# Optimization experiments

Hardware: AMD Instinct MI355X
Metric: run time of the kernel (lower is better)

Reference implementation:

```python
import jax, jax.numpy as jnp
import numpy as np

B, N, DIM = 4, 2048, 512
H, DH = 8, 64  # heads, dim_head; inner_dim = H*DH = 512
SCALE = DH ** -0.5
EPS = 1e-5


def _layer_norm(x, gamma):
    # LayerNorm with learned gamma and beta fixed to zeros (beta is a buffer)
    mu = jnp.mean(x, axis=-1, keepdims=True)
    var = jnp.var(x, axis=-1, keepdims=True)
    return (x - mu) * jax.lax.rsqrt(var + EPS) * gamma


def setup_inputs() -> dict:
    key = jax.random.key(0)
    ks = jax.random.split(key, 6)
    x = jax.random.normal(ks[0], (B, N, DIM), jnp.float32)
    mask = jax.random.bernoulli(ks[1], 0.9, (B, N))  # bool [b, n]
    gamma = jnp.ones((DIM,), jnp.float32)            # pre-attn LayerNorm gamma
    Wq = jax.random.normal(ks[2], (DIM, H * DH), jnp.float32) * 0.02
    Wkv = jax.random.normal(ks[3], (DIM, 2 * DH), jnp.float32) * 0.02  # shared single KV head (MQA)
    null_kv = jax.random.normal(ks[4], (2, DH), jnp.float32)
    Wout = jax.random.normal(ks[5], (H * DH, DIM), jnp.float32) * 0.02
    out_gamma = jnp.ones((DIM,), jnp.float32)        # post-proj LayerNorm gamma
    return {"x": x, "mask": mask, "gamma": gamma, "Wq": Wq, "Wkv": Wkv,
            "null_kv": null_kv, "Wout": Wout, "out_gamma": out_gamma}


def reference(x, mask, gamma, Wq, Wkv, null_kv, Wout, out_gamma):
    b, n, _ = x.shape
    xn = _layer_norm(x, gamma)
    # queries: per-head; keys/values: single shared head (multi-query)
    q = (xn @ Wq).reshape(b, n, H, DH).transpose(0, 2, 1, 3) * SCALE  # [b,h,n,d]
    kv = xn @ Wkv                                                     # [b,n,2d]
    k, v = kv[..., :DH], kv[..., DH:]                                 # [b,n,d]
    # prepend learned null key/value (attention sink) shared across batch
    nk = jnp.broadcast_to(null_kv[0], (b, 1, DH))
    nv = jnp.broadcast_to(null_kv[1], (b, 1, DH))
    k = jnp.concatenate([nk, k], axis=1)  # [b, n+1, d]
    v = jnp.concatenate([nv, v], axis=1)
    sim = jnp.einsum('bhid,bjd->bhij', q, k)  # [b,h,n,n+1]
    # mask padded with True for the null token, broadcast over heads/queries
    m = jnp.concatenate([jnp.ones((b, 1), bool), mask], axis=1)
    max_neg = -jnp.finfo(sim.dtype).max
    sim = jnp.where(m[:, None, None, :], sim, max_neg)
    attn = jax.nn.softmax(sim.astype(jnp.float32), axis=-1).astype(x.dtype)
    out = jnp.einsum('bhij,bjd->bhid', attn, v)       # [b,h,n,d]
    out = out.transpose(0, 2, 1, 3).reshape(b, n, H * DH)
    return _layer_norm(out @ Wout, out_gamma)
```

## Files before the change

### kernel.cpp

```cpp
#include <hip/hip_runtime.h>

typedef __attribute__((ext_vector_type(8)))  short bf16x8;
typedef __attribute__((ext_vector_type(4)))  float f32x4;
typedef __attribute__((ext_vector_type(16))) float f32x16;
typedef __attribute__((ext_vector_type(4)))  unsigned u32x4;

#define Nx 2048
#define CTXx 2049
#define KCAP 2112
#define QSCALE 0.18033688f

__device__ __forceinline__ short f2bs(float x){
    unsigned u = __builtin_bit_cast(unsigned, x);
    u = (u + 0x7fffu + ((u >> 16) & 1u)) >> 16;
    return (short)u;
}
__device__ __forceinline__ unsigned pack_trunc(float a, float b){
    return __builtin_amdgcn_perm(__builtin_bit_cast(unsigned, b),
                                 __builtin_bit_cast(unsigned, a), 0x07060302u);
}

__global__ void __launch_bounds__(256) ln1_prep_kernel(const float* __restrict__ x,
                                                       const float* __restrict__ g,
                                                       short* __restrict__ xnb,
                                                       const float* __restrict__ Wq,
                                                       const float* __restrict__ Wkv,
                                                       const float* __restrict__ Wout,
                                                       const float* __restrict__ nkv,
                                                       short* __restrict__ WcatT,
                                                       short* __restrict__ WoutT,
                                                       short* __restrict__ kb,
                                                       short* __restrict__ vbt){
    __shared__ float ls[64][65];
    int t = threadIdx.x;
    if (blockIdx.x < 2048){
        int w = t >> 6, lane = t & 63;
        size_t row = (size_t)blockIdx.x * 4 + w;
        const float* xr = x + row * 512 + lane * 8;
        float4 a = *(const float4*)xr;
        float4 b = *(const float4*)(xr + 4);
        float s = a.x + a.y + a.z + a.w + b.x + b.y + b.z + b.w;
        float q = a.x*a.x + a.y*a.y + a.z*a.z + a.w*a.w
                + b.x*b.x + b.y*b.y + b.z*b.z + b.w*b.w;
        #pragma unroll
        for (int m = 1; m < 64; m <<= 1){ s += __shfl_xor(s, m, 64); q += __shfl_xor(q, m, 64); }
        float mu  = s * (1.f / 512.f);
        float var = fmaxf(q * (1.f / 512.f) - mu * mu, 0.f);
        float r   = rsqrtf(var + 1e-5f);
        const float* gr = g + lane * 8;
        float4 g0 = *(const float4*)gr;
        float4 g1 = *(const float4*)(gr + 4);
        bf16x8 o;
        o[0] = f2bs((a.x - mu) * r * g0.x); o[1] = f2bs((a.y - mu) * r * g0.y);
        o[2] = f2bs((a.z - mu) * r * g0.z); o[3] = f2bs((a.w - mu) * r * g0.w);
        o[4] = f2bs((b.x - mu) * r * g1.x); o[5] = f2bs((b.y - mu) * r * g1.y);
        o[6] = f2bs((b.z - mu) * r * g1.z); o[7] = f2bs((b.w - mu) * r * g1.w);
        *(bf16x8*)(xnb + row * 512 + lane * 8) = o;
        return;
    }
    int bid = blockIdx.x - 2048;
    if (bid == 144){
        int b = t >> 6, d = t & 63;
        kb[((size_t)b * KCAP) * 64 + d] = f2bs(nkv[d]);
        vbt[((size_t)b * 64 + d) * KCAP + 0] = f2bs(nkv[64 + d]);
        return;
    }
    bool isOut = (bid >= 80);
    int b2 = isOut ? bid - 80 : bid;
    int ntile = isOut ? (b2 & 7) : (b2 % 10);
    int ktile = isOut ? (b2 >> 3) : (b2 / 10);
    int n0 = ntile * 64, k0 = ktile * 64;
    #pragma unroll
    for (int rr = 0; rr < 64; rr += 16){
        int r = rr + (t >> 4), c = (t & 15) * 4;
        float4 v;
        if (isOut)            v = *(const float4*)(Wout + (size_t)(k0 + r) * 512 + n0 + c);
        else if (n0 < 512)    v = *(const float4*)(Wq   + (size_t)(k0 + r) * 512 + n0 + c);
        else                  v = *(const float4*)(Wkv  + (size_t)(k0 + r) * 128 + (n0 - 512) + c);
        ls[c + 0][r] = v.x; ls[c + 1][r] = v.y; ls[c + 2][r] = v.z; ls[c + 3][r] = v.w;
    }
    __syncthreads();
    int rn = t >> 2, kc = (t & 3) * 16;
    short tmp[16];
    #pragma unroll
    for (int j = 0; j < 16; j++) tmp[j] = f2bs(ls[rn][kc + j]);
    short* dst = (isOut ? WoutT : WcatT) + (size_t)(n0 + rn) * 512 + k0 + kc;
    *(int4*)dst       = *(int4*)&tmp[0];
    *(int4*)(dst + 8) = *(int4*)&tmp[8];
}

__global__ void __launch_bounds__(256) ln2_kernel(const float* __restrict__ z,
                                                  const float* __restrict__ g,
                                                  float* __restrict__ out){
    int w = threadIdx.x >> 6, lane = threadIdx.x & 63;
    size_t row = (size_t)blockIdx.x * 4 + w;
    const float* xr = z + row * 512 + lane * 8;
    float4 a = *(const float4*)xr;
    float4 b = *(const float4*)(xr + 4);
    float s = a.x + a.y + a.z + a.w + b.x + b.y + b.z + b.w;
    float q = a.x*a.x + a.y*a.y + a.z*a.z + a.w*a.w
            + b.x*b.x + b.y*b.y + b.z*b.z + b.w*b.w;
    #pragma unroll
    for (int m = 1; m < 64; m <<= 1){ s += __shfl_xor(s, m, 64); q += __shfl_xor(q, m, 64); }
    float mu  = s * (1.f / 512.f);
    float var = fmaxf(q * (1.f / 512.f) - mu * mu, 0.f);
    float r   = rsqrtf(var + 1e-5f);
    const float* gr = g + lane * 8;
    float4 g0 = *(const float4*)gr;
    float4 g1 = *(const float4*)(gr + 4);
    float4 o0, o1;
    o0.x = (a.x - mu) * r * g0.x; o0.y = (a.y - mu) * r * g0.y;
    o0.z = (a.z - mu) * r * g0.z; o0.w = (a.w - mu) * r * g0.w;
    o1.x = (b.x - mu) * r * g1.x; o1.y = (b.y - mu) * r * g1.y;
    o1.z = (b.z - mu) * r * g1.z; o1.w = (b.w - mu) * r * g1.w;
    float* op = out + row * 512 + lane * 8;
    *(float4*)op = o0; *(float4*)(op + 4) = o1;
}

__global__ void __launch_bounds__(256, 1) gemm_qkv(const short* __restrict__ A,
                                                   const short* __restrict__ BwT,
                                                   short* __restrict__ qb,
                                                   short* __restrict__ kb,
                                                   short* __restrict__ vbt){
    __shared__ short As[2][128][72];
    __shared__ short Bs[2][160][72];
    int t = threadIdx.x;
    int lane = t & 63, w = t >> 6;
    int l16 = lane & 15, quad = lane >> 4;
    int wm = w & 1, wn = w >> 1;
    int row0 = blockIdx.y * 128, col0 = blockIdx.x * 160;
    f32x4 acc[4][5];
    #pragma unroll
    for (int i = 0; i < 4; i++)
        #pragma unroll
        for (int j = 0; j < 5; j++) acc[i][j] = (f32x4){0.f, 0.f, 0.f, 0.f};
    int ar = t >> 1, ak = (t & 1) * 32;
    const short* ap = A + (size_t)(row0 + ar) * 512 + ak;
    int4 a0 = *(const int4*)(ap);      int4 a1 = *(const int4*)(ap + 8);
    int4 a2 = *(const int4*)(ap + 16); int4 a3 = *(const int4*)(ap + 24);
    int4 pb[5];
    int brow[5], bseg[5];
    #pragma unroll
    for (int ps = 0; ps < 5; ps++){
        int idx = ps * 256 + t;
        brow[ps] = idx >> 3; bseg[ps] = (idx & 7) * 8;
        pb[ps] = *(const int4*)(BwT + (size_t)(col0 + brow[ps]) * 512 + bseg[ps]);
    }
    int p = 0;
    for (int k0 = 0; k0 < 512; k0 += 64){
        *(int4*)&As[p][ar][ak]      = a0;
        *(int4*)&As[p][ar][ak + 8]  = a1;
        *(int4*)&As[p][ar][ak + 16] = a2;
        *(int4*)&As[p][ar][ak + 24] = a3;
        #pragma unroll
        for (int ps = 0; ps < 5; ps++)
            *(int4*)&Bs[p][brow[ps]][bseg[ps]] = pb[ps];
        __syncthreads();
        int kn = k0 + 64;
        if (kn < 512){
            a0 = *(const int4*)(ap + kn);      a1 = *(const int4*)(ap + kn + 8);
            a2 = *(const int4*)(ap + kn + 16); a3 = *(const int4*)(ap + kn + 24);
            #pragma unroll
            for (int ps = 0; ps < 5; ps++)
                pb[ps] = *(const int4*)(BwT + (size_t)(col0 + brow[ps]) * 512 + kn + bseg[ps]);
        }
        #pragma unroll
        for (int ks = 0; ks < 2; ks++){
            bf16x8 af[4], bfr[5];
            #pragma unroll
            for (int mt = 0; mt < 4; mt++)
                af[mt] = *(const bf16x8*)&As[p][wm * 64 + mt * 16 + l16][ks * 32 + quad * 8];
            #pragma unroll
            for (int nt = 0; nt < 5; nt++)
                bfr[nt] = *(const bf16x8*)&Bs[p][wn * 80 + nt * 16 + l16][ks * 32 + quad * 8];
            #pragma unroll
            for (int mt = 0; mt < 4; mt++)
                #pragma unroll
                for (int nt = 0; nt < 5; nt++)
                    acc[mt][nt] = __builtin_amdgcn_mfma_f32_16x16x32_bf16(af[mt], bfr[nt], acc[mt][nt], 0, 0, 0);
        }
        p ^= 1;
    }
    #pragma unroll
    for (int mt = 0; mt < 4; mt++)
        #pragma unroll
        for (int nt = 0; nt < 5; nt++)
            #pragma unroll
            for (int r = 0; r < 4; r++){
                int row = row0 + wm * 64 + mt * 16 + quad * 4 + r;
                int col = col0 + wn * 80 + nt * 16 + l16;
                float v = acc[mt][nt][r];
                int bb = row >> 11, ii = row & 2047;
                if (col < 512){
                    qb[(size_t)row * 512 + col] = f2bs(v * QSCALE);
                } else if (col < 576){
                    kb[((size_t)bb * KCAP + ii + 1) * 64 + (col - 512)] = f2bs(v);
                } else {
                    vbt[((size_t)bb * 64 + (col - 576)) * KCAP + ii + 1] = f2bs(v);
                }
            }
}

__global__ void __launch_bounds__(256, 2) gemm_out(const short* __restrict__ A,
                                                   const short* __restrict__ BwT,
                                                   float* __restrict__ C){
    __shared__ short As[2][128][72];
    __shared__ short Bs[2][128][72];
    int t = threadIdx.x;
    int lane = t & 63, w = t >> 6;
    int l16 = lane & 15, quad = lane >> 4;
    int wm = w & 1, wn = w >> 1;
    int row0 = blockIdx.y * 128, col0 = blockIdx.x * 128;
    f32x4 acc[4][4];
    #pragma unroll
    for (int i = 0; i < 4; i++)
        #pragma unroll
        for (int j = 0; j < 4; j++) acc[i][j] = (f32x4){0.f, 0.f, 0.f, 0.f};
    int ar = t >> 1, ak = (t & 1) * 32;
    const short* ap = A   + (size_t)(row0 + ar) * 512 + ak;
    const short* bp = BwT + (size_t)(col0 + ar) * 512 + ak;
    int4 a0 = *(const int4*)(ap);      int4 a1 = *(const int4*)(ap + 8);
    int4 a2 = *(const int4*)(ap + 16); int4 a3 = *(const int4*)(ap + 24);
    int4 b0 = *(const int4*)(bp);      int4 b1 = *(const int4*)(bp + 8);
    int4 b2 = *(const int4*)(bp + 16); int4 b3 = *(const int4*)(bp + 24);
    int p = 0;
    for (int k0 = 0; k0 < 512; k0 += 64){
        *(int4*)&As[p][ar][ak]      = a0;
        *(int4*)&As[p][ar][ak + 8]  = a1;
        *(int4*)&As[p][ar][ak + 16] = a2;
        *(int4*)&As[p][ar][ak + 24] = a3;
        *(int4*)&Bs[p][ar][ak]      = b0;
        *(int4*)&Bs[p][ar][ak + 8]  = b1;
        *(int4*)&Bs[p][ar][ak + 16] = b2;
        *(int4*)&Bs[p][ar][ak + 24] = b3;
        __syncthreads();
        int kn = k0 + 64;
        if (kn < 512){
            a0 = *(const int4*)(ap + kn);      a1 = *(const int4*)(ap + kn + 8);
            a2 = *(const int4*)(ap + kn + 16); a3 = *(const int4*)(ap + kn + 24);
            b0 = *(const int4*)(bp + kn);      b1 = *(const int4*)(bp + kn + 8);
            b2 = *(const int4*)(bp + kn + 16); b3 = *(const int4*)(bp + kn + 24);
        }
        #pragma unroll
        for (int ks = 0; ks < 2; ks++){
            bf16x8 af[4], bfr[4];
            #pragma unroll
            for (int mt = 0; mt < 4; mt++)
                af[mt] = *(const bf16x8*)&As[p][wm * 64 + mt * 16 + l16][ks * 32 + quad * 8];
            #pragma unroll
            for (int nt = 0; nt < 4; nt++)
                bfr[nt] = *(const bf16x8*)&Bs[p][wn * 64 + nt * 16 + l16][ks * 32 + quad * 8];
            #pragma unroll
            for (int mt = 0; mt < 4; mt++)
                #pragma unroll
                for (int nt = 0; nt < 4; nt++)
                    acc[mt][nt] = __builtin_amdgcn_mfma_f32_16x16x32_bf16(af[mt], bfr[nt], acc[mt][nt], 0, 0, 0);
        }
        p ^= 1;
    }
    #pragma unroll
    for (int mt = 0; mt < 4; mt++)
        #pragma unroll
        for (int nt = 0; nt < 4; nt++)
            #pragma unroll
            for (int r = 0; r < 4; r++){
                int row = row0 + wm * 64 + mt * 16 + quad * 4 + r;
                int col = col0 + wn * 64 + nt * 16 + l16;
                C[(size_t)row * 512 + col] = acc[mt][nt][r];
            }
}

__global__ void __launch_bounds__(256, 2) attn_kernel(const short* __restrict__ qb,
                                                      const short* __restrict__ kb,
                                                      const short* __restrict__ vbt,
                                                      const int* __restrict__ mask,
                                                      short* __restrict__ ob){
    __shared__ short Ks[2][64][72];
    __shared__ short Vt[2][64][72];
    int t = threadIdx.x;
    int lane = t & 63, w = t >> 6;
    int n32 = lane & 31, hb = lane >> 5;
    int b = blockIdx.y, i0 = blockIdx.x * 16;
    int head = 2 * w + (n32 >> 4), row = i0 + (n32 & 15);
    bf16x8 qf[4];
    {
        const short* qp = qb + ((size_t)(b * Nx + row)) * 512 + head * 64 + hb * 8;
        #pragma unroll
        for (int ks = 0; ks < 4; ks++) qf[ks] = *(const bf16x8*)(qp + ks * 16);
    }
    bf16x8 ones;
    #pragma unroll
    for (int j = 0; j < 8; j++) ones[j] = (short)0x3F80;
    f32x16 oacc[2], lacc;
    #pragma unroll
    for (int j = 0; j < 16; j++){ oacc[0][j] = 0.f; oacc[1][j] = 0.f; lacc[j] = 0.f; }

    int skey = t >> 2, sd = (t & 3) * 16;
    int vd   = t >> 2, vk = (t & 3) * 16;
    const short* kgp = kb  + (size_t)b * KCAP * 64 + skey * 64 + sd;
    const short* vgp = vbt + ((size_t)b * 64 + vd) * KCAP + vk;
    const int* mrow = mask + b * Nx;

    int4 pk0 = *(const int4*)(kgp);
    int4 pk1 = *(const int4*)(kgp + 8);
    int4 pv0 = *(const int4*)(vgp);
    int4 pv1 = *(const int4*)(vgp + 8);
    int mok = (lane == 0) ? 1 : ((lane < CTXx) ? mrow[lane - 1] : 0);

    int p = 0;
    for (int jt = 0; jt < 33; ++jt){
        *(int4*)&Ks[p][skey][sd]     = pk0;
        *(int4*)&Ks[p][skey][sd + 8] = pk1;
        *(int4*)&Vt[p][vd][vk]       = make_int4(pv0.x, pv0.y, pv1.x, pv1.y);
        *(int4*)&Vt[p][vd][vk + 8]   = make_int4(pv0.z, pv0.w, pv1.z, pv1.w);
        unsigned long long bal = __ballot(mok != 0);
        __syncthreads();
        int jn = (jt + 1) * 64;
        if (jt + 1 < 33){
            pk0 = *(const int4*)(kgp + (size_t)jn * 64);
            pk1 = *(const int4*)(kgp + (size_t)jn * 64 + 8);
            pv0 = *(const int4*)(vgp + jn);
            pv1 = *(const int4*)(vgp + jn + 8);
            int jg = jn + lane;
            mok = (jg < CTXx) ? mrow[jg - 1] : 0;
        }
        f32x16 sf[2];
        #pragma unroll
        for (int i = 0; i < 2; i++)
            #pragma unroll
            for (int j = 0; j < 16; j++) sf[i][j] = 0.f;
        #pragma unroll
        for (int ks = 0; ks < 4; ks++){
            #pragma unroll
            for (int kt = 0; kt < 2; kt++){
                bf16x8 kf = *(const bf16x8*)&Ks[p][kt * 32 + n32][ks * 16 + hb * 8];
                sf[kt] = __builtin_amdgcn_mfma_f32_32x32x16_bf16(kf, qf[ks], sf[kt], 0, 0, 0);
            }
        }
        unsigned mlo = (unsigned)(bal >> (4 * hb));
        unsigned mhi = (unsigned)(bal >> (32 + 4 * hb));
        unsigned pg[8][2];
        #pragma unroll
        for (int kt = 0; kt < 2; kt++){
            unsigned mm = kt ? mhi : mlo;
            #pragma unroll
            for (int g4 = 0; g4 < 4; g4++){
                float pr[4];
                #pragma unroll
                for (int tt = 0; tt < 4; tt++){
                    float e = __builtin_amdgcn_exp2f(sf[kt][g4 * 4 + tt]);
                    pr[tt] = ((mm >> (8 * g4 + tt)) & 1u) ? e : 0.f;
                }
                pg[kt * 4 + g4][0] = pack_trunc(pr[0], pr[1]);
                pg[kt * 4 + g4][1] = pack_trunc(pr[2], pr[3]);
            }
        }
        #pragma unroll
        for (int s = 0; s < 4; s++){
            bf16x8 pa = __builtin_bit_cast(bf16x8,
                (u32x4){pg[2 * s][0], pg[2 * s][1], pg[2 * s + 1][0], pg[2 * s + 1][1]});
            lacc = __builtin_amdgcn_mfma_f32_32x32x16_bf16(pa, ones, lacc, 0, 0, 0);
            #pragma unroll
            for (int nt = 0; nt < 2; nt++){
                bf16x8 vf = *(const bf16x8*)&Vt[p][nt * 32 + n32][s * 16 + hb * 8];
                oacc[nt] = __builtin_amdgcn_mfma_f32_32x32x16_bf16(pa, vf, oacc[nt], 0, 0, 0);
            }
        }
        p ^= 1;
    }
    #pragma unroll
    for (int r = 0; r < 16; r++){
        float linv = 1.f / lacc[r];
        int hr = (r & 3) + 8 * (r >> 2) + 4 * hb;
        int grow = i0 + (hr & 15);
        int ghead = 2 * w + (hr >> 4);
        short* op = ob + ((size_t)(b * Nx + grow)) * 512 + ghead * 64 + n32;
        op[0]  = f2bs(oacc[0][r] * linv);
        op[32] = f2bs(oacc[1][r] * linv);
    }
}

extern "C" void kernel_launch(void* const* d_in, const int* in_sizes, int n_in,
                              void* d_out, int out_size, void* d_ws, size_t ws_size,
                              hipStream_t stream){
    const float* x     = (const float*)d_in[0];
    const int*   mask  = (const int*)  d_in[1];
    const float* gamma = (const float*)d_in[2];
    const float* Wq    = (const float*)d_in[3];
    const float* Wkv   = (const float*)d_in[4];
    const float* nkv   = (const float*)d_in[5];
    const float* Wout  = (const float*)d_in[6];
    const float* og    = (const float*)d_in[7];
    float* out = (float*)d_out;

    short* xnb   = (short*)d_ws;
    short* qb    = xnb + (size_t)4194304;
    short* kb    = qb  + (size_t)4194304;
    short* vbt   = kb  + (size_t)540672;
    short* ob    = vbt + (size_t)540672;
    short* WcatT = ob  + (size_t)4194304;
    short* WoutT = WcatT + (size_t)327680;
    float* zb    = (float*)d_ws;

    ln1_prep_kernel<<<2193, 256, 0, stream>>>(x, gamma, xnb, Wq, Wkv, Wout, nkv,
                                              WcatT, WoutT, kb, vbt);
    gemm_qkv    <<<dim3(4, 64), 256, 0, stream>>>(xnb, WcatT, qb, kb, vbt);
    attn_kernel <<<dim3(128, 4), 256, 0, stream>>>(qb, kb, vbt, mask, ob);
    gemm_out    <<<dim3(4, 64), 256, 0, stream>>>(ob, WoutT, zb);
    ln2_kernel  <<<2048, 256, 0, stream>>>(zb, og, out);
}
```

Baseline: 180.2 us.

## Fuse output GEMM with final LayerNorm and drop LDS staging in GEMMs

Both projection GEMMs are rewritten so that each block owns 32 full rows. Each wave loads MFMA fragments straight from global memory with register double-buffering, so LDS tiles and barriers are gone. The output GEMM now computes the row LayerNorm in its epilogue, reducing statistics by shuffle and a small shared array, which removes the fp32 intermediate round trip and the separate ln2 launch. The attention output buffer reuses the xnb workspace. The risk is more redundant global loads of weights per block, uncoalesced direct-to-register loads, and only 256 blocks with one block per CU.

```diff
diff --git a/kernel.cpp b/kernel.cpp
--- a/kernel.cpp
+++ b/kernel.cpp
@@ -89,106 +89,50 @@
     *(int4*)(dst + 8) = *(int4*)&tmp[8];
 }
 
-__global__ void __launch_bounds__(256) ln2_kernel(const float* __restrict__ z,
-                                                  const float* __restrict__ g,
-                                                  float* __restrict__ out){
-    int w = threadIdx.x >> 6, lane = threadIdx.x & 63;
-    size_t row = (size_t)blockIdx.x * 4 + w;
-    const float* xr = z + row * 512 + lane * 8;
-    float4 a = *(const float4*)xr;
-    float4 b = *(const float4*)(xr + 4);
-    float s = a.x + a.y + a.z + a.w + b.x + b.y + b.z + b.w;
-    float q = a.x*a.x + a.y*a.y + a.z*a.z + a.w*a.w
-            + b.x*b.x + b.y*b.y + b.z*b.z + b.w*b.w;
-    #pragma unroll
-    for (int m = 1; m < 64; m <<= 1){ s += __shfl_xor(s, m, 64); q += __shfl_xor(q, m, 64); }
-    float mu  = s * (1.f / 512.f);
-    float var = fmaxf(q * (1.f / 512.f) - mu * mu, 0.f);
-    float r   = rsqrtf(var + 1e-5f);
-    const float* gr = g + lane * 8;
-    float4 g0 = *(const float4*)gr;
-    float4 g1 = *(const float4*)(gr + 4);
-    float4 o0, o1;
-    o0.x = (a.x - mu) * r * g0.x; o0.y = (a.y - mu) * r * g0.y;
-    o0.z = (a.z - mu) * r * g0.z; o0.w = (a.w - mu) * r * g0.w;
-    o1.x = (b.x - mu) * r * g1.x; o1.y = (b.y - mu) * r * g1.y;
-    o1.z = (b.z - mu) * r * g1.z; o1.w = (b.w - mu) * r * g1.w;
-    float* op = out + row * 512 + lane * 8;
-    *(float4*)op = o0; *(float4*)(op + 4) = o1;
-}
-
 __global__ void __launch_bounds__(256, 1) gemm_qkv(const short* __restrict__ A,
                                                    const short* __restrict__ BwT,
                                                    short* __restrict__ qb,
                                                    short* __restrict__ kb,
                                                    short* __restrict__ vbt){
-    __shared__ short As[2][128][72];
-    __shared__ short Bs[2][160][72];
-    int t = threadIdx.x;
-    int lane = t & 63, w = t >> 6;
+    int t = threadIdx.x, lane = t & 63, w = t >> 6;
     int l16 = lane & 15, quad = lane >> 4;
-    int wm = w & 1, wn = w >> 1;
-    int row0 = blockIdx.y * 128, col0 = blockIdx.x * 160;
-    f32x4 acc[4][5];
-    #pragma unroll
-    for (int i = 0; i < 4; i++)
-        #pragma unroll
-        for (int j = 0; j < 5; j++) acc[i][j] = (f32x4){0.f, 0.f, 0.f, 0.f};
-    int ar = t >> 1, ak = (t & 1) * 32;
-    const short* ap = A + (size_t)(row0 + ar) * 512 + ak;
-    int4 a0 = *(const int4*)(ap);      int4 a1 = *(const int4*)(ap + 8);
-    int4 a2 = *(const int4*)(ap + 16); int4 a3 = *(const int4*)(ap + 24);
-    int4 pb[5];
-    int brow[5], bseg[5];
-    #pragma unroll
-    for (int ps = 0; ps < 5; ps++){
-        int idx = ps * 256 + t;
-        brow[ps] = idx >> 3; bseg[ps] = (idx & 7) * 8;
-        pb[ps] = *(const int4*)(BwT + (size_t)(col0 + brow[ps]) * 512 + bseg[ps]);
-    }
-    int p = 0;
-    for (int k0 = 0; k0 < 512; k0 += 64){
-        *(int4*)&As[p][ar][ak]      = a0;
-        *(int4*)&As[p][ar][ak + 8]  = a1;
-        *(int4*)&As[p][ar][ak + 16] = a2;
-        *(int4*)&As[p][ar][ak + 24] = a3;
-        #pragma unroll
-        for (int ps = 0; ps < 5; ps++)
-            *(int4*)&Bs[p][brow[ps]][bseg[ps]] = pb[ps];
-        __syncthreads();
-        int kn = k0 + 64;
-        if (kn < 512){
-            a0 = *(const int4*)(ap + kn);      a1 = *(const int4*)(ap + kn + 8);
-            a2 = *(const int4*)(ap + kn + 16); a3 = *(const int4*)(ap + kn + 24);
-            #pragma unroll
-            for (int ps = 0; ps < 5; ps++)
-                pb[ps] = *(const int4*)(BwT + (size_t)(col0 + brow[ps]) * 512 + kn + bseg[ps]);
-        }
-        #pragma unroll
-        for (int ks = 0; ks < 2; ks++){
-            bf16x8 af[4], bfr[5];
-            #pragma unroll
-            for (int mt = 0; mt < 4; mt++)
-                af[mt] = *(const bf16x8*)&As[p][wm * 64 + mt * 16 + l16][ks * 32 + quad * 8];
-            #pragma unroll
-            for (int nt = 0; nt < 5; nt++)
-                bfr[nt] = *(const bf16x8*)&Bs[p][wn * 80 + nt * 16 + l16][ks * 32 + quad * 8];
-            #pragma unroll
-            for (int mt = 0; mt < 4; mt++)
-                #pragma unroll
-                for (int nt = 0; nt < 5; nt++)
-                    acc[mt][nt] = __builtin_amdgcn_mfma_f32_16x16x32_bf16(af[mt], bfr[nt], acc[mt][nt], 0, 0, 0);
-        }
-        p ^= 1;
-    }
-    #pragma unroll
-    for (int mt = 0; mt < 4; mt++)
-        #pragma unroll
-        for (int nt = 0; nt < 5; nt++)
+    int row0 = blockIdx.x * 32;
+    const short* aB = A   + (size_t)(row0 + l16) * 512 + quad * 8;
+    const short* bB = BwT + (size_t)(w * 160 + l16) * 512 + quad * 8;
+    f32x4 acc[2][10];
+    #pragma unroll
+    for (int mt = 0; mt < 2; mt++)
+        #pragma unroll
+        for (int nt = 0; nt < 10; nt++) acc[mt][nt] = (f32x4){0.f, 0.f, 0.f, 0.f};
+    bf16x8 af[2][2], bf[2][10];
+    #pragma unroll
+    for (int mt = 0; mt < 2; mt++) af[0][mt] = *(const bf16x8*)(aB + mt * 8192);
+    #pragma unroll
+    for (int nt = 0; nt < 10; nt++) bf[0][nt] = *(const bf16x8*)(bB + nt * 8192);
+    #pragma unroll
+    for (int it = 0; it < 16; ++it){
+        int cur = it & 1, nxt = cur ^ 1;
+        if (it < 15){
+            int kn = (it + 1) * 32;
+            #pragma unroll
+            for (int mt = 0; mt < 2; mt++) af[nxt][mt] = *(const bf16x8*)(aB + mt * 8192 + kn);
+            #pragma unroll
+            for (int nt = 0; nt < 10; nt++) bf[nxt][nt] = *(const bf16x8*)(bB + nt * 8192 + kn);
+        }
+        #pragma unroll
+        for (int mt = 0; mt < 2; mt++)
+            #pragma unroll
+            for (int nt = 0; nt < 10; nt++)
+                acc[mt][nt] = __builtin_amdgcn_mfma_f32_16x16x32_bf16(af[cur][mt], bf[cur][nt], acc[mt][nt], 0, 0, 0);
+    }
+    #pragma unroll
+    for (int mt = 0; mt < 2; mt++)
+        #pragma unroll
+        for (int nt = 0; nt < 10; nt++)
             #pragma unroll
             for (int r = 0; r < 4; r++){
-                int row = row0 + wm * 64 + mt * 16 + quad * 4 + r;
-                int col = col0 + wn * 80 + nt * 16 + l16;
+                int row = row0 + mt * 16 + quad * 4 + r;
+                int col = w * 160 + nt * 16 + l16;
                 float v = acc[mt][nt][r];
                 int bb = row >> 11, ii = row & 2047;
                 if (col < 512){
@@ -201,73 +145,77 @@
             }
 }
 
-__global__ void __launch_bounds__(256, 2) gemm_out(const short* __restrict__ A,
-                                                   const short* __restrict__ BwT,
-                                                   float* __restrict__ C){
-    __shared__ short As[2][128][72];
-    __shared__ short Bs[2][128][72];
-    int t = threadIdx.x;
-    int lane = t & 63, w = t >> 6;
+__global__ void __launch_bounds__(256, 1) gemm_out_ln2(const short* __restrict__ A,
+                                                       const short* __restrict__ BwT,
+                                                       const float* __restrict__ og,
+                                                       float* __restrict__ out){
+    __shared__ float Sred[4][32], Qred[4][32];
+    int t = threadIdx.x, lane = t & 63, w = t >> 6;
     int l16 = lane & 15, quad = lane >> 4;
-    int wm = w & 1, wn = w >> 1;
-    int row0 = blockIdx.y * 128, col0 = blockIdx.x * 128;
-    f32x4 acc[4][4];
-    #pragma unroll
-    for (int i = 0; i < 4; i++)
-        #pragma unroll
-        for (int j = 0; j < 4; j++) acc[i][j] = (f32x4){0.f, 0.f, 0.f, 0.f};
-    int ar = t >> 1, ak = (t & 1) * 32;
-    const short* ap = A   + (size_t)(row0 + ar) * 512 + ak;
-    const short* bp = BwT + (size_t)(col0 + ar) * 512 + ak;
-    int4 a0 = *(const int4*)(ap);      int4 a1 = *(const int4*)(ap + 8);
-    int4 a2 = *(const int4*)(ap + 16); int4 a3 = *(const int4*)(ap + 24);
-    int4 b0 = *(const int4*)(bp);      int4 b1 = *(const int4*)(bp + 8);
-    int4 b2 = *(const int4*)(bp + 16); int4 b3 = *(const int4*)(bp + 24);
-    int p = 0;
-    for (int k0 = 0; k0 < 512; k0 += 64){
-        *(int4*)&As[p][ar][ak]      = a0;
-        *(int4*)&As[p][ar][ak + 8]  = a1;
-        *(int4*)&As[p][ar][ak + 16] = a2;
-        *(int4*)&As[p][ar][ak + 24] = a3;
-        *(int4*)&Bs[p][ar][ak]      = b0;
-        *(int4*)&Bs[p][ar][ak + 8]  = b1;
-        *(int4*)&Bs[p][ar][ak + 16] = b2;
-        *(int4*)&Bs[p][ar][ak + 24] = b3;
-        __syncthreads();
-        int kn = k0 + 64;
-        if (kn < 512){
-            a0 = *(const int4*)(ap + kn);      a1 = *(const int4*)(ap + kn + 8);
-            a2 = *(const int4*)(ap + kn + 16); a3 = *(const int4*)(ap + kn + 24);
-            b0 = *(const int4*)(bp + kn);      b1 = *(const int4*)(bp + kn + 8);
-            b2 = *(const int4*)(bp + kn + 16); b3 = *(const int4*)(bp + kn + 24);
-        }
-        #pragma unroll
-        for (int ks = 0; ks < 2; ks++){
-            bf16x8 af[4], bfr[4];
-            #pragma unroll
-            for (int mt = 0; mt < 4; mt++)
-                af[mt] = *(const bf16x8*)&As[p][wm * 64 + mt * 16 + l16][ks * 32 + quad * 8];
-            #pragma unroll
-            for (int nt = 0; nt < 4; nt++)
-                bfr[nt] = *(const bf16x8*)&Bs[p][wn * 64 + nt * 16 + l16][ks * 32 + quad * 8];
-            #pragma unroll
-            for (int mt = 0; mt < 4; mt++)
-                #pragma unroll
-                for (int nt = 0; nt < 4; nt++)
-                    acc[mt][nt] = __builtin_amdgcn_mfma_f32_16x16x32_bf16(af[mt], bfr[nt], acc[mt][nt], 0, 0, 0);
-        }
-        p ^= 1;
-    }
-    #pragma unroll
-    for (int mt = 0; mt < 4; mt++)
-        #pragma unroll
-        for (int nt = 0; nt < 4; nt++)
-            #pragma unroll
-            for (int r = 0; r < 4; r++){
-                int row = row0 + wm * 64 + mt * 16 + quad * 4 + r;
-                int col = col0 + wn * 64 + nt * 16 + l16;
-                C[(size_t)row * 512 + col] = acc[mt][nt][r];
-            }
+    int row0 = blockIdx.x * 32;
+    const short* aB = A   + (size_t)(row0 + l16) * 512 + quad * 8;
+    const short* bB = BwT + (size_t)(w * 128 + l16) * 512 + quad * 8;
+    f32x4 acc[2][8];
+    #pragma unroll
+    for (int mt = 0; mt < 2; mt++)
+        #pragma unroll
+        for (int nt = 0; nt < 8; nt++) acc[mt][nt] = (f32x4){0.f, 0.f, 0.f, 0.f};
+    bf16x8 af[2][2], bf[2][8];
+    #pragma unroll
+    for (int mt = 0; mt < 2; mt++) af[0][mt] = *(const bf16x8*)(aB + mt * 8192);
+    #pragma unroll
+    for (int nt = 0; nt < 8; nt++) bf[0][nt] = *(const bf16x8*)(bB + nt * 8192);
+    #pragma unroll
+    for (int it = 0; it < 16; ++it){
+        int cur = it & 1, nxt = cur ^ 1;
+        if (it < 15){
+            int kn = (it + 1) * 32;
+            #pragma unroll
+            for (int mt = 0; mt < 2; mt++) af[nxt][mt] = *(const bf16x8*)(aB + mt * 8192 + kn);
+            #pragma unroll
+            for (int nt = 0; nt < 8; nt++) bf[nxt][nt] = *(const bf16x8*)(bB + nt * 8192 + kn);
+        }
+        #pragma unroll
+        for (int mt = 0; mt < 2; mt++)
+            #pragma unroll
+            for (int nt = 0; nt < 8; nt++)
+                acc[mt][nt] = __builtin_amdgcn_mfma_f32_16x16x32_bf16(af[cur][mt], bf[cur][nt], acc[mt][nt], 0, 0, 0);
+    }
+    #pragma unroll
+    for (int mt = 0; mt < 2; mt++)
+        #pragma unroll
+        for (int r = 0; r < 4; r++){
+            float s = 0.f, q = 0.f;
+            #pragma unroll
+            for (int nt = 0; nt < 8; nt++){
+                float v = acc[mt][nt][r];
+                s += v; q += v * v;
+            }
+            #pragma unroll
+            for (int m = 1; m < 16; m <<= 1){ s += __shfl_xor(s, m, 64); q += __shfl_xor(q, m, 64); }
+            if (l16 == 0){
+                int rl = mt * 16 + quad * 4 + r;
+                Sred[w][rl] = s; Qred[w][rl] = q;
+            }
+        }
+    __syncthreads();
+    #pragma unroll
+    for (int mt = 0; mt < 2; mt++)
+        #pragma unroll
+        for (int r = 0; r < 4; r++){
+            int rl = mt * 16 + quad * 4 + r;
+            float S = Sred[0][rl] + Sred[1][rl] + Sred[2][rl] + Sred[3][rl];
+            float Q = Qred[0][rl] + Qred[1][rl] + Qred[2][rl] + Qred[3][rl];
+            float mu  = S * (1.f / 512.f);
+            float var = fmaxf(Q * (1.f / 512.f) - mu * mu, 0.f);
+            float rstd = rsqrtf(var + 1e-5f);
+            float* op = out + (size_t)(row0 + rl) * 512;
+            #pragma unroll
+            for (int nt = 0; nt < 8; nt++){
+                int col = w * 128 + nt * 16 + l16;
+                op[col] = (acc[mt][nt][r] - mu) * rstd * og[col];
+            }
+        }
 }
 
 __global__ void __launch_bounds__(256, 2) attn_kernel(const short* __restrict__ qb,
@@ -397,15 +345,13 @@
     short* qb    = xnb + (size_t)4194304;
     short* kb    = qb  + (size_t)4194304;
     short* vbt   = kb  + (size_t)540672;
-    short* ob    = vbt + (size_t)540672;
-    short* WcatT = ob  + (size_t)4194304;
+    short* WcatT = vbt + (size_t)540672;
     short* WoutT = WcatT + (size_t)327680;
-    float* zb    = (float*)d_ws;
+    short* ob    = xnb;
 
     ln1_prep_kernel<<<2193, 256, 0, stream>>>(x, gamma, xnb, Wq, Wkv, Wout, nkv,
                                               WcatT, WoutT, kb, vbt);
-    gemm_qkv    <<<dim3(4, 64), 256, 0, stream>>>(xnb, WcatT, qb, kb, vbt);
+    gemm_qkv    <<<256, 256, 0, stream>>>(xnb, WcatT, qb, kb, vbt);
     attn_kernel <<<dim3(128, 4), 256, 0, stream>>>(qb, kb, vbt, mask, ob);
-    gemm_out    <<<dim3(4, 64), 256, 0, stream>>>(ob, WoutT, zb);
-    ln2_kernel  <<<2048, 256, 0, stream>>>(zb, og, out);
-}
+    gemm_out_ln2<<<256, 256, 0, stream>>>(ob, WoutT, og, out);
+}
```

New measurement: 182.4 us. Within noise of the previous version (+1.2%).
